# Optimization experiments

Measured on AMD Instinct MI355X. Metric: run time of the kernel, lower is better.

The kernel has to match this reference:

```python
import jax, jax.numpy as jnp
import numpy as np

N_NODES = 50000
N_EDGES = 800000
D_FEAT = 64      # input_size
D_OUT = 64       # output_size
N_REL = 8
N_BASES = 4


def setup_inputs() -> dict:
    key = jax.random.key(0)
    k1, k2, k3, k4, k5, k6 = jax.random.split(key, 6)
    x = jax.random.normal(k1, (N_NODES, D_FEAT, N_REL), dtype=jnp.float32)
    edge_src = jax.random.randint(k2, (N_EDGES,), 0, N_NODES, dtype=jnp.int32)
    edge_dst = jax.random.randint(k3, (N_EDGES,), 0, N_NODES, dtype=jnp.int32)
    edge_weight = jax.random.uniform(k4, (N_EDGES,), dtype=jnp.float32)
    # basis-decomposed relation weights (xavier-like scale)
    w_bases = jax.random.normal(k5, (N_BASES, D_FEAT, D_OUT), dtype=jnp.float32) * (2.0 / (D_FEAT + D_OUT)) ** 0.5
    w_rel = jax.random.normal(k6, (N_REL, N_BASES), dtype=jnp.float32) * (2.0 / (N_REL + N_BASES)) ** 0.5
    return {"x": x, "edge_src": edge_src, "edge_dst": edge_dst,
            "edge_weight": edge_weight, "w_bases": w_bases, "w_rel": w_rel}


def reference(x, edge_src, edge_dst, edge_weight, w_bases, w_rel):
    # w[r] = sum_b w_rel[r,b] * w_bases[b]  -> [R, d_in, d_out]
    w = jnp.einsum('rb,bio->rio', w_rel, w_bases)
    n_rel = x.shape[-1]
    n_nodes = x.shape[0]
    # sparse adjacency message passing per relation: support_r = A @ x[:, :, r]
    # A @ y == segment_sum over edges (dst <- weight * y[src])
    supports = []
    for r in range(n_rel):  # small fixed relation count
        msgs = edge_weight[:, None] * x[edge_src, :, r]          # [E, d_in]
        agg = jax.ops.segment_sum(msgs, edge_dst, num_segments=n_nodes)  # [N, d_in]
        supports.append(agg)
    tmp = jnp.concatenate(supports, axis=1)                      # [N, R*d_in]
    weights = w.reshape(n_rel * x.shape[1], w.shape[2])          # [R*d_in, d_out]
    out = tmp @ weights                                          # [N, d_out]
    return out
```

## Files before the change

### kernel.cpp

```cpp
#include <hip/hip_runtime.h>
#include <hip/hip_bf16.h>

#define DFEAT   64
#define NREL    8
#define KDIM    512
#define DOUT    64
#define NBASES  4

__global__ __launch_bounds__(256) void weight_kernel(
    const float* __restrict__ w_rel,
    const float* __restrict__ w_bases,
    float* __restrict__ wflat,
    int* __restrict__ cnt, int n_nodes)
{
    int idx = blockIdx.x * 256 + threadIdx.x;
    int o = idx & 63;
    int k = idx >> 6;
    int i = k >> 3;
    int r = k & 7;
    float s = 0.f;
#pragma unroll
    for (int b = 0; b < NBASES; ++b)
        s += w_rel[r * NBASES + b] * w_bases[(b * DFEAT + i) * DOUT + o];
    wflat[idx] = s;

    for (int j = idx; j < n_nodes; j += KDIM * DOUT)
        cnt[j] = 0;
}

#define BN   64
#define BK   32
#define XSS  36

__global__ __launch_bounds__(256) void fused_kernel(
    const float* __restrict__ x,
    const float* __restrict__ w,
    float* __restrict__ y,
    int n_nodes,
    const int* __restrict__ esrc, const int* __restrict__ edst,
    const float* __restrict__ ew,
    int* __restrict__ cnt, int2* __restrict__ bucket,
    int n_edges, int cap, int t_blocks, int p_threads)
{
    __shared__ float xs[BN][XSS];
    __shared__ float ws[BK][DOUT];

    const int tid = threadIdx.x;

    if (blockIdx.x >= t_blocks) {
        int e0 = (blockIdx.x - t_blocks) * 256 + tid;
        for (int e = e0; e < n_edges; e += p_threads) {
            int d = edst[e];
            int pos = atomicAdd(&cnt[d], 1);
            if (pos < cap) {
                bucket[(size_t)d * cap + pos] =
                    make_int2(esrc[e], __float_as_int(ew[e]));
            }
        }
        return;
    }

    const int node0 = blockIdx.x * BN;

    const int tn = tid >> 4;
    const int to = tid & 15;

    const int ln = tid >> 2;
    const int lk = (tid & 3) * 8;

    int xrow = node0 + ln;
    if (xrow >= n_nodes) xrow = n_nodes - 1;
    const float* xg = x + (size_t)xrow * KDIM;

    float acc[4][4];
#pragma unroll
    for (int a = 0; a < 4; ++a)
#pragma unroll
        for (int b = 0; b < 4; ++b) acc[a][b] = 0.f;

    for (int kb = 0; kb < KDIM; kb += BK) {
        float4 xa = *(const float4*)(xg + kb + lk);
        float4 xb = *(const float4*)(xg + kb + lk + 4);
        float4 wa = *(const float4*)(w + kb * DOUT + tid * 4);
        float4 wb = *(const float4*)(w + kb * DOUT + 1024 + tid * 4);

        __syncthreads();
        *(float4*)&xs[ln][lk]     = xa;
        *(float4*)&xs[ln][lk + 4] = xb;
        *(float4*)(&ws[0][0] + tid * 4)        = wa;
        *(float4*)(&ws[0][0] + 1024 + tid * 4) = wb;
        __syncthreads();

#pragma unroll
        for (int kk = 0; kk < BK; kk += 4) {
            float4 xv[4], wv[4];
#pragma unroll
            for (int a = 0; a < 4; ++a)
                xv[a] = *(const float4*)&xs[tn * 4 + a][kk];
#pragma unroll
            for (int j = 0; j < 4; ++j)
                wv[j] = *(const float4*)&ws[kk + j][to * 4];
#pragma unroll
            for (int a = 0; a < 4; ++a) {
                float xr[4] = {xv[a].x, xv[a].y, xv[a].z, xv[a].w};
#pragma unroll
                for (int j = 0; j < 4; ++j) {
                    float wr[4] = {wv[j].x, wv[j].y, wv[j].z, wv[j].w};
                    acc[a][0] += xr[j] * wr[0];
                    acc[a][1] += xr[j] * wr[1];
                    acc[a][2] += xr[j] * wr[2];
                    acc[a][3] += xr[j] * wr[3];
                }
            }
        }
    }

#pragma unroll
    for (int a = 0; a < 4; ++a) {
        int node = node0 + tn * 4 + a;
        if (node < n_nodes) {
            float4 v = make_float4(acc[a][0], acc[a][1], acc[a][2], acc[a][3]);
            *(float4*)(y + (size_t)node * DOUT + to * 4) = v;
        }
    }
}

__global__ __launch_bounds__(256) void gather_kernel(
    const int* __restrict__ cnt, const int2* __restrict__ bucket,
    const float* __restrict__ y,
    float* __restrict__ out, int n_nodes, int cap)
{
    int node = blockIdx.x * 4 + (threadIdx.x >> 6);
    int lane = threadIdx.x & 63;
    int sub = lane >> 4;
    int fi  = lane & 15;
    if (node >= n_nodes) return;

    int deg = cnt[node];
    if (deg > cap) deg = cap;
    const int2* b = bucket + (size_t)node * cap;

    float4 acc = make_float4(0.f, 0.f, 0.f, 0.f);
    for (int e = sub; e < deg; e += 4) {
        int2 sv = b[e];
        float wgt = __int_as_float(sv.y);
        float4 yv = *(const float4*)(y + (size_t)sv.x * DOUT + fi * 4);
        acc.x += wgt * yv.x;
        acc.y += wgt * yv.y;
        acc.z += wgt * yv.z;
        acc.w += wgt * yv.w;
    }

#pragma unroll
    for (int mask = 16; mask <= 32; mask <<= 1) {
        acc.x += __shfl_xor(acc.x, mask);
        acc.y += __shfl_xor(acc.y, mask);
        acc.z += __shfl_xor(acc.z, mask);
        acc.w += __shfl_xor(acc.w, mask);
    }

    if (sub == 0)
        *(float4*)(out + (size_t)node * DOUT + fi * 4) = acc;
}

extern "C" void kernel_launch(void* const* d_in, const int* in_sizes, int n_in,
                              void* d_out, int out_size, void* d_ws, size_t ws_size,
                              hipStream_t stream) {
    const float* x       = (const float*)d_in[0];
    const int*   esrc    = (const int*)d_in[1];
    const int*   edst    = (const int*)d_in[2];
    const float* ew      = (const float*)d_in[3];
    const float* w_bases = (const float*)d_in[4];
    const float* w_rel   = (const float*)d_in[5];
    float* out = (float*)d_out;

    const int n_nodes = in_sizes[0] / KDIM;
    const int n_edges = in_sizes[1];

    size_t base_elems = (size_t)n_nodes * DOUT + KDIM * DOUT + n_nodes;
    int cap = 64;
    while (cap > 16 && (base_elems + (size_t)n_nodes * cap * 2) * 4 > ws_size)
        cap -= 16;

    float* y      = (float*)d_ws;
    float* wflat  = y + (size_t)n_nodes * DOUT;
    int*   cnt    = (int*)(wflat + KDIM * DOUT);
    int2*  bucket = (int2*)(cnt + n_nodes);

    weight_kernel<<<(KDIM * DOUT) / 256, 256, 0, stream>>>(
        w_rel, w_bases, wflat, cnt, n_nodes);

    const int t_blocks = (n_nodes + BN - 1) / BN;
    const int p_blocks = 1024;
    fused_kernel<<<t_blocks + p_blocks, 256, 0, stream>>>(
        x, wflat, y, n_nodes,
        esrc, edst, ew, cnt, bucket, n_edges, cap,
        t_blocks, p_blocks * 256);

    int gblocks = (n_nodes + 3) / 4;
    gather_kernel<<<gblocks, 256, 0, stream>>>(cnt, bucket, y, out, n_nodes, cap);
}
```

Measured before the change: 236.2 us.

## Use bf16 MFMA for node transform and shuffle-broadcast bucket entries in gather

Replaces the fp32 LDS-tiled FMA GEMM with per-wave bf16 MFMA 16x16x32, converting x rows to bf16 in registers and storing the combined weight pre-transposed in bf16. This removes the shared-memory staging and block barriers. The gather now loads each node's bucket entries once per lane and broadcasts them with shuffles, and it uses two accumulators for more memory-level parallelism. Bf16 rounding of x and the weights lowers precision. The gather also assumes cap is at most 64.

```diff
diff --git a/kernel.cpp b/kernel.cpp
--- a/kernel.cpp
+++ b/kernel.cpp
@@ -7,34 +7,39 @@
 #define DOUT    64
 #define NBASES  4
 
+typedef short short8 __attribute__((ext_vector_type(8)));
+typedef float f32x4  __attribute__((ext_vector_type(4)));
+
+__device__ __forceinline__ short f2bf(float f) {
+    unsigned u = __float_as_uint(f);
+    u += 0x7fff + ((u >> 16) & 1);
+    return (short)(u >> 16);
+}
+
 __global__ __launch_bounds__(256) void weight_kernel(
     const float* __restrict__ w_rel,
     const float* __restrict__ w_bases,
-    float* __restrict__ wflat,
+    short* __restrict__ wT,
     int* __restrict__ cnt, int n_nodes)
 {
     int idx = blockIdx.x * 256 + threadIdx.x;
-    int o = idx & 63;
-    int k = idx >> 6;
+    int k = idx & 511;
+    int o = idx >> 9;
     int i = k >> 3;
     int r = k & 7;
     float s = 0.f;
 #pragma unroll
     for (int b = 0; b < NBASES; ++b)
         s += w_rel[r * NBASES + b] * w_bases[(b * DFEAT + i) * DOUT + o];
-    wflat[idx] = s;
+    wT[o * KDIM + k] = f2bf(s);
 
     for (int j = idx; j < n_nodes; j += KDIM * DOUT)
         cnt[j] = 0;
 }
 
-#define BN   64
-#define BK   32
-#define XSS  36
-
 __global__ __launch_bounds__(256) void fused_kernel(
     const float* __restrict__ x,
-    const float* __restrict__ w,
+    const short* __restrict__ wT,
     float* __restrict__ y,
     int n_nodes,
     const int* __restrict__ esrc, const int* __restrict__ edst,
@@ -42,9 +47,6 @@
     int* __restrict__ cnt, int2* __restrict__ bucket,
     int n_edges, int cap, int t_blocks, int p_threads)
 {
-    __shared__ float xs[BN][XSS];
-    __shared__ float ws[BK][DOUT];
-
     const int tid = threadIdx.x;
 
     if (blockIdx.x >= t_blocks) {
@@ -60,67 +62,52 @@
         return;
     }
 
-    const int node0 = blockIdx.x * BN;
-
-    const int tn = tid >> 4;
-    const int to = tid & 15;
-
-    const int ln = tid >> 2;
-    const int lk = (tid & 3) * 8;
-
-    int xrow = node0 + ln;
-    if (xrow >= n_nodes) xrow = n_nodes - 1;
-    const float* xg = x + (size_t)xrow * KDIM;
-
-    float acc[4][4];
+    const int wid  = tid >> 6;
+    const int lane = tid & 63;
+    const int quad = lane >> 4;
+    const int fi   = lane & 15;
+
+    const int node0 = (blockIdx.x * 4 + wid) * 16;
+    if (node0 >= n_nodes) return;
+
+    int myrow = node0 + fi;
+    if (myrow >= n_nodes) myrow = n_nodes - 1;
+    const float* xg = x + (size_t)myrow * KDIM + quad * 8;
+    const short* wg = wT + fi * KDIM + quad * 8;
+
+    f32x4 acc0 = {0.f, 0.f, 0.f, 0.f};
+    f32x4 acc1 = {0.f, 0.f, 0.f, 0.f};
+    f32x4 acc2 = {0.f, 0.f, 0.f, 0.f};
+    f32x4 acc3 = {0.f, 0.f, 0.f, 0.f};
+
+#pragma unroll 4
+    for (int kb = 0; kb < KDIM; kb += 32) {
+        float4 xa = *(const float4*)(xg + kb);
+        float4 xb = *(const float4*)(xg + kb + 4);
+        short8 a;
+        a[0] = f2bf(xa.x); a[1] = f2bf(xa.y); a[2] = f2bf(xa.z); a[3] = f2bf(xa.w);
+        a[4] = f2bf(xb.x); a[5] = f2bf(xb.y); a[6] = f2bf(xb.z); a[7] = f2bf(xb.w);
+
+        short8 b0 = *(const short8*)(wg + kb);
+        short8 b1 = *(const short8*)(wg + 16 * KDIM + kb);
+        short8 b2 = *(const short8*)(wg + 32 * KDIM + kb);
+        short8 b3 = *(const short8*)(wg + 48 * KDIM + kb);
+
+        acc0 = __builtin_amdgcn_mfma_f32_16x16x32_bf16(a, b0, acc0, 0, 0, 0);
+        acc1 = __builtin_amdgcn_mfma_f32_16x16x32_bf16(a, b1, acc1, 0, 0, 0);
+        acc2 = __builtin_amdgcn_mfma_f32_16x16x32_bf16(a, b2, acc2, 0, 0, 0);
+        acc3 = __builtin_amdgcn_mfma_f32_16x16x32_bf16(a, b3, acc3, 0, 0, 0);
+    }
+
 #pragma unroll
-    for (int a = 0; a < 4; ++a)
-#pragma unroll
-        for (int b = 0; b < 4; ++b) acc[a][b] = 0.f;
-
-    for (int kb = 0; kb < KDIM; kb += BK) {
-        float4 xa = *(const float4*)(xg + kb + lk);
-        float4 xb = *(const float4*)(xg + kb + lk + 4);
-        float4 wa = *(const float4*)(w + kb * DOUT + tid * 4);
-        float4 wb = *(const float4*)(w + kb * DOUT + 1024 + tid * 4);
-
-        __syncthreads();
-        *(float4*)&xs[ln][lk]     = xa;
-        *(float4*)&xs[ln][lk + 4] = xb;
-        *(float4*)(&ws[0][0] + tid * 4)        = wa;
-        *(float4*)(&ws[0][0] + 1024 + tid * 4) = wb;
-        __syncthreads();
-
-#pragma unroll
-        for (int kk = 0; kk < BK; kk += 4) {
-            float4 xv[4], wv[4];
-#pragma unroll
-            for (int a = 0; a < 4; ++a)
-                xv[a] = *(const float4*)&xs[tn * 4 + a][kk];
-#pragma unroll
-            for (int j = 0; j < 4; ++j)
-                wv[j] = *(const float4*)&ws[kk + j][to * 4];
-#pragma unroll
-            for (int a = 0; a < 4; ++a) {
-                float xr[4] = {xv[a].x, xv[a].y, xv[a].z, xv[a].w};
-#pragma unroll
-                for (int j = 0; j < 4; ++j) {
-                    float wr[4] = {wv[j].x, wv[j].y, wv[j].z, wv[j].w};
-                    acc[a][0] += xr[j] * wr[0];
-                    acc[a][1] += xr[j] * wr[1];
-                    acc[a][2] += xr[j] * wr[2];
-                    acc[a][3] += xr[j] * wr[3];
-                }
-            }
-        }
-    }
-
-#pragma unroll
-    for (int a = 0; a < 4; ++a) {
-        int node = node0 + tn * 4 + a;
+    for (int r = 0; r < 4; ++r) {
+        int node = node0 + quad * 4 + r;
         if (node < n_nodes) {
-            float4 v = make_float4(acc[a][0], acc[a][1], acc[a][2], acc[a][3]);
-            *(float4*)(y + (size_t)node * DOUT + to * 4) = v;
+            float* yr = y + (size_t)node * DOUT + fi;
+            yr[0]  = acc0[r];
+            yr[16] = acc1[r];
+            yr[32] = acc2[r];
+            yr[48] = acc3[r];
         }
     }
 }
@@ -138,19 +125,30 @@
 
     int deg = cnt[node];
     if (deg > cap) deg = cap;
-    const int2* b = bucket + (size_t)node * cap;
-
-    float4 acc = make_float4(0.f, 0.f, 0.f, 0.f);
-    for (int e = sub; e < deg; e += 4) {
-        int2 sv = b[e];
-        float wgt = __int_as_float(sv.y);
-        float4 yv = *(const float4*)(y + (size_t)sv.x * DOUT + fi * 4);
-        acc.x += wgt * yv.x;
-        acc.y += wgt * yv.y;
-        acc.z += wgt * yv.z;
-        acc.w += wgt * yv.w;
-    }
-
+
+    int src = 0; float wgt = 0.f;
+    if (lane < deg) {
+        int2 sv = bucket[(size_t)node * cap + lane];
+        src = sv.x;
+        wgt = __int_as_float(sv.y);
+    }
+
+    float4 acc0 = make_float4(0.f, 0.f, 0.f, 0.f);
+    float4 acc1 = make_float4(0.f, 0.f, 0.f, 0.f);
+    for (int c = 0; c < deg; c += 8) {
+        int e0 = c + sub, e1 = c + 4 + sub;
+        int   s0 = __shfl(src, e0), s1 = __shfl(src, e1);
+        float w0 = __shfl(wgt, e0), w1 = __shfl(wgt, e1);
+        float4 y0 = *(const float4*)(y + (size_t)s0 * DOUT + fi * 4);
+        float4 y1 = *(const float4*)(y + (size_t)s1 * DOUT + fi * 4);
+        acc0.x += w0 * y0.x; acc0.y += w0 * y0.y;
+        acc0.z += w0 * y0.z; acc0.w += w0 * y0.w;
+        acc1.x += w1 * y1.x; acc1.y += w1 * y1.y;
+        acc1.z += w1 * y1.z; acc1.w += w1 * y1.w;
+    }
+
+    float4 acc = make_float4(acc0.x + acc1.x, acc0.y + acc1.y,
+                             acc0.z + acc1.z, acc0.w + acc1.w);
 #pragma unroll
     for (int mask = 16; mask <= 32; mask <<= 1) {
         acc.x += __shfl_xor(acc.x, mask);
@@ -177,23 +175,23 @@
     const int n_nodes = in_sizes[0] / KDIM;
     const int n_edges = in_sizes[1];
 
-    size_t base_elems = (size_t)n_nodes * DOUT + KDIM * DOUT + n_nodes;
+    size_t base_words = (size_t)n_nodes * DOUT + (KDIM * DOUT) / 2 + n_nodes;
     int cap = 64;
-    while (cap > 16 && (base_elems + (size_t)n_nodes * cap * 2) * 4 > ws_size)
+    while (cap > 16 && (base_words + (size_t)n_nodes * cap * 2) * 4 > ws_size)
         cap -= 16;
 
     float* y      = (float*)d_ws;
-    float* wflat  = y + (size_t)n_nodes * DOUT;
-    int*   cnt    = (int*)(wflat + KDIM * DOUT);
+    short* wT     = (short*)(y + (size_t)n_nodes * DOUT);
+    int*   cnt    = (int*)(wT + KDIM * DOUT);
     int2*  bucket = (int2*)(cnt + n_nodes);
 
     weight_kernel<<<(KDIM * DOUT) / 256, 256, 0, stream>>>(
-        w_rel, w_bases, wflat, cnt, n_nodes);
-
-    const int t_blocks = (n_nodes + BN - 1) / BN;
+        w_rel, w_bases, wT, cnt, n_nodes);
+
+    const int t_blocks = (n_nodes + 63) / 64;
     const int p_blocks = 1024;
     fused_kernel<<<t_blocks + p_blocks, 256, 0, stream>>>(
-        x, wflat, y, n_nodes,
+        x, wT, y, n_nodes,
         esrc, edst, ew, cnt, bucket, n_edges, cap,
         t_blocks, p_blocks * 256);
 
```

Measured after the change: 239.8 us. About the same (+1.5%).
